# Performance work log

Measured on AMD Instinct MI355X. Metric: run time of the kernel, lower is better.

The kernel has to match this reference:

```python
import jax, jax.numpy as jnp
import numpy as np

B, C, D, H, W = 8, 96, 8, 32, 32
HW, DIM, NH = H * W, C * D, 4
DH = DIM // NH
EPS_NORM = 1e-12
EPS_LN = 1e-5


def setup_inputs() -> dict:
    key = jax.random.key(0)
    ks = jax.random.split(key, 10)
    s = 0.02
    return {
        "x": jax.random.normal(ks[0], (B, C, D, H, W), jnp.float32),
        "pos_embed": jax.random.normal(ks[1], (1, HW, DIM), jnp.float32) * s,
        "qkv_w": jax.random.normal(ks[2], (3 * DIM, DIM), jnp.float32) * s,
        "proj_w": jax.random.normal(ks[3], (DIM, DIM), jnp.float32) * s,
        "proj_b": jnp.zeros((DIM,), jnp.float32),
        "temperature": jnp.ones((NH, 1, 1), jnp.float32),
        "ln_gamma": jnp.ones((DIM,), jnp.float32),
        "ln_beta": jnp.zeros((DIM,), jnp.float32),
        "dw_w": jax.random.normal(ks[4], (C, 1, 3, 3, 3), jnp.float32) * s,
        "dw_b": jnp.zeros((C,), jnp.float32),
        "pw_w": jax.random.normal(ks[5], (C, C, 1, 1, 1), jnp.float32) * s,
        "pw_b": jnp.zeros((C,), jnp.float32),
    }


def _l2norm_seq(t):
    # normalize over the HW axis (dim=-2), matching F.normalize(dim=-2)
    n = jnp.sqrt(jnp.sum(t * t, axis=-2, keepdims=True))
    return t / jnp.maximum(n, EPS_NORM)


def _dsconv(y, dw_w, dw_b, pw_w, pw_b):
    dn = ("NCDHW", "OIDHW", "NCDHW")
    z = jax.lax.conv_general_dilated(y, dw_w, (1, 1, 1), [(1, 1)] * 3,
                                     dimension_numbers=dn, feature_group_count=C)
    z = z + dw_b[None, :, None, None, None]
    z = jax.lax.conv_general_dilated(z, pw_w, (1, 1, 1), [(0, 0)] * 3,
                                     dimension_numbers=dn)
    return z + pw_b[None, :, None, None, None]


def reference(x, pos_embed, qkv_w, proj_w, proj_b, temperature,
              ln_gamma, ln_beta, dw_w, dw_b, pw_w, pw_b):
    save = x
    # b c d h w -> b (h w) (c d)
    t = jnp.transpose(x, (0, 3, 4, 1, 2)).reshape(B, HW, DIM)
    t = t + pos_embed
    # qkv projection (no bias)
    qkv = (t @ qkv_w.T).reshape(B, HW, 3, NH, DH)
    qkv = jnp.transpose(qkv, (2, 0, 3, 1, 4))  # [3,B,NH,HW,DH]
    q, k, v = qkv[0], qkv[1], qkv[2]
    q = _l2norm_seq(q)
    k = _l2norm_seq(k)
    attn = jnp.einsum("bhnd,bhmd->bhnm", q, k) * temperature  # temp broadcasts [NH,1,1]
    attn = jax.nn.softmax(attn, axis=-1)  # dropout = identity at eval
    o = jnp.einsum("bhnm,bhmd->bhnd", attn, v)
    o = jnp.transpose(o, (0, 2, 1, 3)).reshape(B, HW, DIM)
    o = o @ proj_w.T + proj_b
    # LayerNorm applied to attention output
    mu = jnp.mean(o, axis=-1, keepdims=True)
    var = jnp.mean((o - mu) ** 2, axis=-1, keepdims=True)
    o = (o - mu) / jnp.sqrt(var + EPS_LN) * ln_gamma + ln_beta
    # b (h w) (c d) -> b c d h w
    o = o.reshape(B, H, W, C, D)
    o = jnp.transpose(o, (0, 3, 4, 1, 2))
    y = o + save
    return y + _dsconv(y, dw_w, dw_b, pw_w, pw_b)
```

## Files before the change

### kernel.cpp

```cpp
#include <hip/hip_runtime.h>

typedef unsigned short u16;
typedef unsigned int u32;

typedef __attribute__((ext_vector_type(8))) short short8;
typedef __attribute__((ext_vector_type(4))) float floatx4;

__device__ __forceinline__ float bf2f(u16 u) { return __uint_as_float(((u32)u) << 16); }
__device__ __forceinline__ u16 f2bf(float f) {
    u32 x = __float_as_uint(f);
    x += 0x7fffu + ((x >> 16) & 1u);
    return (u16)(x >> 16);
}
__device__ __forceinline__ void gl_lds16(const void* g, void* l) {
    __builtin_amdgcn_global_load_lds((const __attribute__((address_space(1))) u32*)g,
                                     (__attribute__((address_space(3))) u32*)l, 16, 0, 0);
}


__global__ __launch_bounds__(256) void k_init(const float* __restrict__ x,
                                              const float* __restrict__ pos,
                                              const float* __restrict__ wq,
                                              const float* __restrict__ wp,
                                              const float* __restrict__ wpw,
                                              u16* __restrict__ t,
                                              u16* __restrict__ wout,
                                              float* __restrict__ zbuf) {
    __shared__ float tile[64][65];
    const int bid = blockIdx.x;
    const int tid = threadIdx.x;
    if (bid < 1536) {
        const int cd0 = (bid % 12) * 64;
        const int hw0 = ((bid / 12) & 15) * 64;
        const int b = bid / 192;
#pragma unroll
        for (int i = 0; i < 16; i++) {
            int f = i * 256 + tid;
            int cdl = f >> 6, hwl = f & 63;
            int cd = cd0 + cdl, c = cd >> 3, d = cd & 7;
            tile[cdl][hwl] = x[(size_t)(((b * 96 + c) * 8 + d)) * 1024 + hw0 + hwl];
        }
        __syncthreads();
#pragma unroll
        for (int it = 0; it < 2; it++) {
            int u = it * 256 + tid;
            int ch = u >> 6, l = u & 63;
            int n16l = ch >> 1, kcl = ch & 1;
            int hwl = n16l * 16 + (l & 15);
            int cdl = kcl * 32 + (l >> 4) * 8;
            int row = b * 1024 + hw0 + hwl;
            int cd = cd0 + cdl;
            const float* pp = pos + (size_t)(hw0 + hwl) * 768 + cd;
            float4 p0 = *(const float4*)pp;
            float4 p1 = *(const float4*)(pp + 4);
            short8 v;
            v[0] = (short)f2bf(tile[cdl + 0][hwl] + p0.x);
            v[1] = (short)f2bf(tile[cdl + 1][hwl] + p0.y);
            v[2] = (short)f2bf(tile[cdl + 2][hwl] + p0.z);
            v[3] = (short)f2bf(tile[cdl + 3][hwl] + p0.w);
            v[4] = (short)f2bf(tile[cdl + 4][hwl] + p1.x);
            v[5] = (short)f2bf(tile[cdl + 5][hwl] + p1.y);
            v[6] = (short)f2bf(tile[cdl + 6][hwl] + p1.z);
            v[7] = (short)f2bf(tile[cdl + 7][hwl] + p1.w);
            size_t chunk = (size_t)(row >> 4) * 24 + (cd >> 5);
            *(short8*)(t + chunk * 512 + l * 8) = v;
        }
    } else if (bid < 2724) {
        const int NQ = 144 * 24 * 64;
        const int NP = NQ + 48 * 24 * 64;
        int u = (bid - 1536) * 256 + tid;
        if (u < NP) {
            const float* w = (u < NQ) ? wq : wp;
            int ub = (u < NQ) ? u : u - NQ;
            int chunk = ub >> 6, l = ub & 63;
            int n16 = chunk / 24, kc = chunk - n16 * 24;
            int n = n16 * 16 + (l & 15);
            int k0 = kc * 32 + (l >> 4) * 8;
            const float* src = w + (size_t)n * 768 + k0;
            float4 a = *(const float4*)src;
            float4 b2 = *(const float4*)(src + 4);
            short8 v;
            v[0] = (short)f2bf(a.x);  v[1] = (short)f2bf(a.y);
            v[2] = (short)f2bf(a.z);  v[3] = (short)f2bf(a.w);
            v[4] = (short)f2bf(b2.x); v[5] = (short)f2bf(b2.y);
            v[6] = (short)f2bf(b2.z); v[7] = (short)f2bf(b2.w);
            *(short8*)(wout + (size_t)u * 8) = v;
        } else {
            int i = u - NP;
            wout[(size_t)NP * 8 + i] = f2bf(wpw[i]);
        }
    } else {
        int i = (bid - 2724) * 256 + tid;
        zbuf[i] = 0.f;
    }
}

template <int MODE>
__global__ __launch_bounds__(256) void gemm_bt(const u16* __restrict__ A,
                                               const u16* __restrict__ Bw,
                                               int M, int N, int K,
                                               u16* __restrict__ qo, u16* __restrict__ ko,
                                               u16* __restrict__ vo,
                                               const float* __restrict__ bias,
                                               u16* __restrict__ Co,
                                               float* __restrict__ sqa,
                                               float* __restrict__ ska,
                                               float* __restrict__ musum,
                                               float* __restrict__ sqsum) {
    __shared__ __align__(16) u16 lAB[128 * 136];
    u16* lA = lAB;
    u16* lB = lAB + 16 * 512;
    const int tid = threadIdx.x;
    const int lane = tid & 63;
    const int wv = tid >> 6;
    const int wr = wv >> 1, wc = wv & 1;
    const int ntiles = N >> 7;
    const int mtiles = M >> 7;
    const int lin = blockIdx.x;
    const int xcd = lin & 7;
    const int idx = lin >> 3;
    const int mlocal = idx / ntiles;
    const int ntile = idx - mlocal * ntiles;
    const int m0 = (xcd * (mtiles >> 3) + mlocal) << 7;
    const int n0 = ntile << 7;
    const int lr = lane & 15;
    const int lq = lane >> 4;

    floatx4 acc[4][4];
#pragma unroll
    for (int i = 0; i < 4; i++)
#pragma unroll
        for (int j = 0; j < 4; j++) acc[i][j] = (floatx4){0.f, 0.f, 0.f, 0.f};

    const int m16 = m0 >> 4, n16 = n0 >> 4;
    for (int kc2 = 0; kc2 < (K >> 6); kc2++) {
        __syncthreads();
#pragma unroll
        for (int kh = 0; kh < 2; kh++) {
#pragma unroll
            for (int i = 0; i < 2; i++) {
                int ch16 = i * 4 + wv;
                int kc = kc2 * 2 + kh;
                const u16* ga = A + ((size_t)(m16 + ch16) * 24 + kc) * 512 + lane * 8;
                gl_lds16(ga, (char*)lA + (kh * 8 + ch16) * 1024);
                const u16* gb = Bw + ((size_t)(n16 + ch16) * 24 + kc) * 512 + lane * 8;
                gl_lds16(gb, (char*)lB + (kh * 8 + ch16) * 1024);
            }
        }
        __syncthreads();
#pragma unroll
        for (int kh = 0; kh < 2; kh++) {
            short8 af[4], bfr[4];
#pragma unroll
            for (int tt = 0; tt < 4; tt++) {
                af[tt] = *(const short8*)(lA + ((kh * 8 + wr * 4 + tt) * 64 + lane) * 8);
                bfr[tt] = *(const short8*)(lB + ((kh * 8 + wc * 4 + tt) * 64 + lane) * 8);
            }
#pragma unroll
            for (int mt = 0; mt < 4; mt++)
#pragma unroll
                for (int nt = 0; nt < 4; nt++)
                    acc[mt][nt] = __builtin_amdgcn_mfma_f32_16x16x32_bf16(af[mt], bfr[nt], acc[mt][nt], 0, 0, 0);
        }
    }

    if (MODE == 0) {
        const int region = n0 / 768;
        const int n0r = n0 - region * 768;
        const int bb0 = m0 >> 10;
        if (region < 2) {
            float* dst = (region == 0) ? sqa : ska;
#pragma unroll
            for (int nt = 0; nt < 4; nt++) {
                int colb = n0r + wc * 64 + nt * 16;
                int h = colb / 192;
                int dh = colb - h * 192 + lr;
                float s = 0.f;
#pragma unroll
                for (int mt = 0; mt < 4; mt++)
#pragma unroll
                    for (int r = 0; r < 4; r++) s += acc[mt][nt][r] * acc[mt][nt][r];
                s += __shfl_xor(s, 16);
                s += __shfl_xor(s, 32);
                if (lq == 0) atomicAdd(&dst[(bb0 * 4 + h) * 192 + dh], s);
            }
        }
        __syncthreads();
        if (region < 2) {
#pragma unroll
            for (int nt = 0; nt < 4; nt++) {
                int lch = wc * 2 + (nt >> 1);
                int offbase = (((nt & 1) * 2 + (lr >> 3)) * 16) * 8 + (lr & 7);
#pragma unroll
                for (int mt = 0; mt < 4; mt++) {
                    u16* cp2 = lAB + (((wr * 4 + mt) * 4 + lch) * 512);
#pragma unroll
                    for (int r = 0; r < 4; r++)
                        cp2[offbase + (lq * 4 + r) * 8] = f2bf(acc[mt][nt][r]);
                }
            }
        } else {
#pragma unroll
            for (int nt = 0; nt < 4; nt++) {
#pragma unroll
                for (int mt = 0; mt < 4; mt++) {
                    u16* cp2 = lAB + (((wr * 2 + (mt >> 1)) * 8 + wc * 4 + nt) * 512);
                    int ob = (((mt & 1) * 2 + (lq >> 1)) * 16 + lr) * 8 + (lq & 1) * 4;
#pragma unroll
                    for (int r = 0; r < 4; r++)
                        cp2[ob + r] = f2bf(acc[mt][nt][r]);
                }
            }
        }
        __syncthreads();
        const int b = m0 >> 10;
        const int ml = m0 & 1023;
        u16* dsto = (region == 0) ? qo : (region == 1) ? ko : vo;
#pragma unroll
        for (int i = 0; i < 8; i++) {
            int ci = wv * 8 + i;
            short8 val = *(const short8*)(lAB + ci * 512 + lane * 8);
            if (region < 2) {
                int a = ci >> 2, bb = ci & 3;
                int cg = n0r + bb * 32;
                int h = cg / 192;
                int dh32 = (cg - h * 192) >> 5;
                size_t gaddr = (size_t)(b * 4 + h) * 196608 +
                               (size_t)((((ml >> 4) + a) * 6 + dh32)) * 512 + lane * 8;
                *(short8*)(dsto + gaddr) = val;
            } else {
                int a = ci >> 3, bb = ci & 7;
                int cg = n0r + bb * 16;
                int h = cg / 192;
                int dh16 = (cg - h * 192) >> 4;
                size_t gaddr = (size_t)(b * 4 + h) * 196608 +
                               (size_t)((((ml >> 5) + a) * 12 + dh16)) * 512 + lane * 8;
                *(short8*)(dsto + gaddr) = val;
            }
        }
    } else {
        float bvv[4];
#pragma unroll
        for (int nt = 0; nt < 4; nt++) bvv[nt] = bias[n0 + wc * 64 + nt * 16 + lr];
#pragma unroll
        for (int mt = 0; mt < 4; mt++) {
#pragma unroll
            for (int r = 0; r < 4; r++) {
                float s = 0.f, ss = 0.f;
#pragma unroll
                for (int nt = 0; nt < 4; nt++) {
                    float v = acc[mt][nt][r] + bvv[nt];
                    s += v;
                    ss += v * v;
                }
#pragma unroll
                for (int m = 1; m < 16; m <<= 1) {
                    s += __shfl_xor(s, m);
                    ss += __shfl_xor(ss, m);
                }
                if (lr == 0) {
                    int row = m0 + wr * 64 + mt * 16 + lq * 4 + r;
                    atomicAdd(&musum[row], s);
                    atomicAdd(&sqsum[row], ss);
                }
            }
        }
        __syncthreads();
#pragma unroll
        for (int nt = 0; nt < 4; nt++) {
            int coll = wc * 64 + nt * 16 + lr;
#pragma unroll
            for (int mt = 0; mt < 4; mt++) {
#pragma unroll
                for (int r = 0; r < 4; r++) {
                    int rowl = wr * 64 + mt * 16 + lq * 4 + r;
                    lAB[rowl * 136 + coll] = f2bf(acc[mt][nt][r] + bvv[nt]);
                }
            }
        }
        __syncthreads();
#pragma unroll
        for (int i = 0; i < 8; i++) {
            int u = i * 256 + tid;
            int rowl = u >> 4, l = u & 15;
            short8 val = *(const short8*)(lAB + rowl * 136 + l * 8);
            *(short8*)(Co + (size_t)(m0 + rowl) * N + n0 + l * 8) = val;
        }
    }
}

__global__ __launch_bounds__(128) void k_attn(const u16* __restrict__ q,
                                              const u16* __restrict__ kmat,
                                              const u16* __restrict__ vT,
                                              const float* __restrict__ sqq,
                                              const float* __restrict__ sqk,
                                              const float* __restrict__ temp,
                                              u16* __restrict__ o) {
    __shared__ __align__(16) u16 lK[24 * 512];
    __shared__ __align__(16) u16 lV[24 * 512];
    __shared__ __align__(16) u16 lP[2 * 2048];
    __shared__ float lcs[192];
    const int lin = blockIdx.x;
    const int qb = (lin >> 3) & 15;
    const int bh = (lin & 7) * 4 + (lin >> 7);
    const int b = bh >> 2, h = bh & 3;
    const int tid = threadIdx.x;
    const int lane = tid & 63;
    const int wv = tid >> 6;
    const int lr = lane & 15;
    const int lq = lane >> 4;
    const int koff = lq * 8;

    const u16* qbase = q + (size_t)bh * 196608;
    const u16* kbase = kmat + (size_t)bh * 196608;
    const u16* vbase = vT + (size_t)bh * 196608;

    {
        const float tv = temp[bh & 3];
        for (int i = tid; i < 192; i += 128) {
            float rq = 1.f / fmaxf(sqrtf(sqq[bh * 192 + i]), 1e-12f);
            float rk = 1.f / fmaxf(sqrtf(sqk[bh * 192 + i]), 1e-12f);
            lcs[i] = rq * rk * tv;
        }
    }
    __syncthreads();

    short8 qf[2][6];
#pragma unroll
    for (int t = 0; t < 2; t++) {
        const int qr16 = qb * 4 + wv * 2 + t;
#pragma unroll
        for (int ks = 0; ks < 6; ks++) {
            short8 raw = *(const short8*)(qbase + ((size_t)(qr16 * 6 + ks)) * 512 + (size_t)lane * 8);
            short8 sc;
#pragma unroll
            for (int j = 0; j < 8; j++) {
                float f = bf2f((u16)raw[j]) * lcs[ks * 32 + koff + j];
                sc[j] = (short)f2bf(f);
            }
            qf[t][ks] = sc;
        }
    }

    float l_r[2][4];
    floatx4 oacc[2][12];
#pragma unroll
    for (int t = 0; t < 2; t++) {
#pragma unroll
        for (int r = 0; r < 4; r++) l_r[t][r] = 0.f;
#pragma unroll
        for (int vt = 0; vt < 12; vt++) oacc[t][vt] = (floatx4){0.f, 0.f, 0.f, 0.f};
    }

    u16* lp = lP + wv * 2048;

    auto stage_K = [&](int kb2) {
#pragma unroll
        for (int i = 0; i < 12; i++) {
            int ch = i * 2 + wv;
            int ks = ch >> 2, nt = ch & 3;
            const u16* gk = kbase + ((size_t)(kb2 * 4 + nt) * 6 + ks) * 512 + lane * 8;
            gl_lds16(gk, (char*)lK + ch * 1024);
        }
    };
    auto stage_V = [&](int kb2) {
#pragma unroll
        for (int i = 0; i < 12; i++) {
            int ch = i * 2 + wv;
            int ks2 = ch / 12, vt2 = ch - ks2 * 12;
            const u16* gv = vbase + ((size_t)(kb2 * 2 + ks2) * 12 + vt2) * 512 + lane * 8;
            gl_lds16(gv, (char*)lV + ch * 1024);
        }
    };

    asm volatile("s_waitcnt vmcnt(0)" ::: "memory");
    stage_K(0);
    stage_V(0);
    asm volatile("s_waitcnt vmcnt(12)" ::: "memory");
    __builtin_amdgcn_s_barrier();

    for (int kb = 0; kb < 16; kb++) {
        floatx4 s0[4], s1[4];
#pragma unroll
        for (int nt = 0; nt < 4; nt++) {
            s0[nt] = (floatx4){0.f, 0.f, 0.f, 0.f};
            s1[nt] = (floatx4){0.f, 0.f, 0.f, 0.f};
        }
        __builtin_amdgcn_s_setprio(1);
#pragma unroll
        for (int ks = 0; ks < 6; ks++) {
#pragma unroll
            for (int nt = 0; nt < 4; nt++) {
                short8 kf = *(const short8*)(lK + ((ks * 4 + nt) * 64 + lane) * 8);
                s0[nt] = __builtin_amdgcn_mfma_f32_16x16x32_bf16(qf[0][ks], kf, s0[nt], 0, 0, 0);
                s1[nt] = __builtin_amdgcn_mfma_f32_16x16x32_bf16(qf[1][ks], kf, s1[nt], 0, 0, 0);
            }
        }
        __builtin_amdgcn_s_setprio(0);
        __builtin_amdgcn_s_barrier();
        if (kb < 15) stage_K(kb + 1);

        float rs0[4] = {0.f, 0.f, 0.f, 0.f}, rs1[4] = {0.f, 0.f, 0.f, 0.f};
#pragma unroll
        for (int nt = 0; nt < 4; nt++)
#pragma unroll
            for (int r = 0; r < 4; r++) {
                float p0 = __expf(s0[nt][r]);
                s0[nt][r] = p0;
                rs0[r] += p0;
                float p1 = __expf(s1[nt][r]);
                s1[nt][r] = p1;
                rs1[r] += p1;
            }
#pragma unroll
        for (int m = 1; m < 16; m <<= 1)
#pragma unroll
            for (int r = 0; r < 4; r++) {
                rs0[r] += __shfl_xor(rs0[r], m);
                rs1[r] += __shfl_xor(rs1[r], m);
            }
#pragma unroll
        for (int r = 0; r < 4; r++) {
            l_r[0][r] += rs0[r];
            l_r[1][r] += rs1[r];
        }
#pragma unroll
        for (int nt = 0; nt < 4; nt++) {
            int base2 = (nt >> 1) * 512 + ((nt & 1) * 2 + (lr >> 3)) * 128 + (lr & 7);
#pragma unroll
            for (int r = 0; r < 4; r++) {
                lp[base2 + (lq * 4 + r) * 8] = f2bf(s0[nt][r]);
                lp[1024 + base2 + (lq * 4 + r) * 8] = f2bf(s1[nt][r]);
            }
        }

        if (kb < 15) { asm volatile("s_waitcnt vmcnt(12)" ::: "memory"); }
        else         { asm volatile("s_waitcnt vmcnt(0)" ::: "memory"); }
        __builtin_amdgcn_s_barrier();

        __builtin_amdgcn_s_setprio(1);
#pragma unroll
        for (int ks2 = 0; ks2 < 2; ks2++) {
            short8 pf0 = *(const short8*)(lp + ks2 * 512 + lane * 8);
            short8 pf1 = *(const short8*)(lp + 1024 + ks2 * 512 + lane * 8);
#pragma unroll
            for (int vt = 0; vt < 12; vt++) {
                short8 vf = *(const short8*)(lV + ((ks2 * 12 + vt) * 64 + lane) * 8);
                oacc[0][vt] = __builtin_amdgcn_mfma_f32_16x16x32_bf16(pf0, vf, oacc[0][vt], 0, 0, 0);
                oacc[1][vt] = __builtin_amdgcn_mfma_f32_16x16x32_bf16(pf1, vf, oacc[1][vt], 0, 0, 0);
            }
        }
        __builtin_amdgcn_s_setprio(0);
        __builtin_amdgcn_s_barrier();
        if (kb < 15) {
            stage_V(kb + 1);
            asm volatile("s_waitcnt vmcnt(12)" ::: "memory");
            __builtin_amdgcn_s_barrier();
        }
    }

    __syncthreads();
#pragma unroll
    for (int t = 0; t < 2; t++) {
        float inv[4];
#pragma unroll
        for (int r = 0; r < 4; r++) inv[r] = 1.f / l_r[t][r];
#pragma unroll
        for (int vt = 0; vt < 12; vt++) {
            int col = vt * 16 + lr;
            int swb = (col >> 5) * 512 + (((col >> 3) & 3) * 16) * 8 + (col & 7);
#pragma unroll
            for (int r = 0; r < 4; r++) {
                int rowl = wv * 32 + t * 16 + lq * 4 + r;
                lK[(rowl >> 4) * 3072 + swb + (rowl & 15) * 8] = f2bf(oacc[t][vt][r] * inv[r]);
            }
        }
    }
    __syncthreads();
#pragma unroll
    for (int i = 0; i < 12; i++) {
        int u = i * 128 + tid;
        int chl = u >> 6, l = u & 63;
        short8 val = *(const short8*)(lK + chl * 512 + l * 8);
        int a = chl / 6, kc = chl - a * 6;
        size_t gaddr = ((size_t)(b * 64 + qb * 4 + a) * 24 + h * 6 + kc) * 512 + l * 8;
        *(short8*)(o + gaddr) = val;
    }
}

__global__ __launch_bounds__(256) void k_lnt(const u16* __restrict__ o2,
                                             const float* __restrict__ musum,
                                             const float* __restrict__ sqsum,
                                             const float* __restrict__ gamma,
                                             const float* __restrict__ beta,
                                             const float* __restrict__ x,
                                             float* __restrict__ y) {
    __shared__ float tile[64][65];
    const int b = blockIdx.z, hw0 = blockIdx.y * 64, cd0 = blockIdx.x * 64;
    const int tid = threadIdx.x;
#pragma unroll
    for (int i = 0; i < 16; i++) {
        int f = i * 256 + tid;
        int hwl = f >> 6, cdl = f & 63;
        int row = b * 1024 + hw0 + hwl;
        float m_ = musum[row] * (1.f / 768.f);
        float var = fmaxf(sqsum[row] * (1.f / 768.f) - m_ * m_, 0.f);
        float rstd = rsqrtf(var + 1e-5f);
        float v = bf2f(o2[(size_t)row * 768 + cd0 + cdl]);
        v = (v - m_) * rstd * gamma[cd0 + cdl] + beta[cd0 + cdl];
        tile[hwl][cdl] = v;
    }
    __syncthreads();
#pragma unroll
    for (int i = 0; i < 16; i++) {
        int f = i * 256 + tid;
        int cdl = f >> 6, hwl = f & 63;
        int cd = cd0 + cdl, c = cd >> 3, d = cd & 7;
        size_t addr = (size_t)((b * 96 + c) * 8 + d) * 1024 + hw0 + hwl;
        y[addr] = tile[hwl][cdl] + x[addr];
    }
}

__global__ __launch_bounds__(256) void k_dw(const float* __restrict__ y,
                                            const float* __restrict__ w,
                                            const float* __restrict__ bias,
                                            u16* __restrict__ z) {
    __shared__ float ly[8192];
    const int bc = blockIdx.x;
    const int c = bc % 96;
    const int tid = threadIdx.x;
    const size_t base = (size_t)bc * 8192;

#pragma unroll
    for (int i = 0; i < 8; i++) {
        int i4 = i * 256 + tid;
        *(float4*)(ly + i4 * 4) = *(const float4*)(y + base + i4 * 4);
    }
    float wt[27];
#pragma unroll
    for (int j = 0; j < 27; j++) wt[j] = w[c * 27 + j];
    const float bv = bias[c];
    __syncthreads();

    const int wcol = tid & 31;
    const int hh = tid >> 5;

    for (int hb = 0; hb < 4; hb++) {
        const int h = hb * 8 + hh;
        float pl[3][9];
        auto loadplane = [&](int dd, float* p) {
#pragma unroll
            for (int kh = 0; kh < 3; kh++) {
                int h2 = h + kh - 1;
                bool hok = (unsigned)h2 < 32u;
                const float* row = ly + dd * 1024 + h2 * 32;
#pragma unroll
                for (int kw = 0; kw < 3; kw++) {
                    int w2 = wcol + kw - 1;
                    bool ok = hok && (unsigned)w2 < 32u;
                    p[kh * 3 + kw] = ok ? row[w2] : 0.f;
                }
            }
        };
#pragma unroll
        for (int j = 0; j < 9; j++) pl[0][j] = 0.f;
        loadplane(0, pl[1]);
#pragma unroll
        for (int d = 0; d < 8; d++) {
            if (d < 7) loadplane(d + 1, pl[2]);
            else {
#pragma unroll
                for (int j = 0; j < 9; j++) pl[2][j] = 0.f;
            }
            float acc = bv;
#pragma unroll
            for (int kd = 0; kd < 3; kd++)
#pragma unroll
                for (int j = 0; j < 9; j++) acc += wt[kd * 9 + j] * pl[kd][j];
            z[base + d * 1024 + h * 32 + wcol] = f2bf(acc);
#pragma unroll
            for (int j = 0; j < 9; j++) { pl[0][j] = pl[1][j]; pl[1][j] = pl[2][j]; }
        }
    }
}

__global__ __launch_bounds__(256) void k_pw(const u16* __restrict__ z,
                                            const u16* __restrict__ wbf,
                                            const float* __restrict__ bias,
                                            float* __restrict__ out) {
    __shared__ __align__(16) u16 lZ[128 * 104];
    __shared__ __align__(16) u16 lW[96 * 104];
    const int tid = threadIdx.x;
    const int lane = tid & 63;
    const int wv = tid >> 6;
    const int lr = lane & 15;
    const int lq = lane >> 4;
    const int koff = lq * 8;

    const int idx = blockIdx.x;
    const int q = idx & 7;
    const int bd = idx >> 3;
    const int b = bd >> 3, d = bd & 7;
    const int pos0 = q * 128;

    for (int i = tid; i < 96 * 96; i += 256) {
        int row = i / 96, col = i - row * 96;
        lW[row * 104 + col] = wbf[i];
    }
    {
        const int pos = tid & 127;
        const int cc0 = (tid >> 7) * 48;
        const size_t gbase = ((size_t)b * 96 * 8 + d) * 1024 + pos0 + pos;
#pragma unroll
        for (int g = 0; g < 6; g++) {
            short8 v;
#pragma unroll
            for (int j = 0; j < 8; j++) {
                int cc = cc0 + g * 8 + j;
                v[j] = (short)z[gbase + (size_t)cc * 8192];
            }
            *(short8*)(lZ + pos * 104 + cc0 + g * 8) = v;
        }
    }
    __syncthreads();

    floatx4 acc[6][2];
#pragma unroll
    for (int m = 0; m < 6; m++)
#pragma unroll
        for (int nt = 0; nt < 2; nt++) acc[m][nt] = (floatx4){0.f, 0.f, 0.f, 0.f};

#pragma unroll
    for (int ks = 0; ks < 3; ks++) {
        short8 bfrg[2];
#pragma unroll
        for (int nt = 0; nt < 2; nt++)
            bfrg[nt] = *(const short8*)(lZ + (wv * 32 + nt * 16 + lr) * 104 + ks * 32 + koff);
#pragma unroll
        for (int m = 0; m < 6; m++) {
            short8 afr = *(const short8*)(lW + (m * 16 + lr) * 104 + ks * 32 + koff);
#pragma unroll
            for (int nt = 0; nt < 2; nt++)
                acc[m][nt] = __builtin_amdgcn_mfma_f32_16x16x32_bf16(afr, bfrg[nt], acc[m][nt], 0, 0, 0);
        }
    }

#pragma unroll
    for (int m = 0; m < 6; m++) {
#pragma unroll
        for (int r = 0; r < 4; r++) {
            int c = m * 16 + lq * 4 + r;
            float bv = bias[c];
            size_t rowbase = ((size_t)(b * 96 + c) * 8 + d) * 1024 + pos0;
#pragma unroll
            for (int nt = 0; nt < 2; nt++) {
                int pos = wv * 32 + nt * 16 + lr;
                size_t a = rowbase + pos;
                out[a] = out[a] + bv + acc[m][nt][r];
            }
        }
    }
}

extern "C" void kernel_launch(void* const* d_in, const int* in_sizes, int n_in,
                              void* d_out, int out_size, void* d_ws, size_t ws_size,
                              hipStream_t stream) {
    (void)in_sizes; (void)n_in; (void)out_size; (void)ws_size;
    const float* x      = (const float*)d_in[0];
    const float* pos    = (const float*)d_in[1];
    const float* qkv_w  = (const float*)d_in[2];
    const float* proj_w = (const float*)d_in[3];
    const float* proj_b = (const float*)d_in[4];
    const float* temp   = (const float*)d_in[5];
    const float* ln_g   = (const float*)d_in[6];
    const float* ln_b   = (const float*)d_in[7];
    const float* dw_w   = (const float*)d_in[8];
    const float* dw_b   = (const float*)d_in[9];
    const float* pw_w   = (const float*)d_in[10];
    const float* pw_b   = (const float*)d_in[11];
    float* out = (float*)d_out;
    char* ws = (char*)d_ws;

    u16* t    = (u16*)(ws + 0);
    u16* vT   = (u16*)(ws + 12582912);
    u16* q    = (u16*)(ws + 25165824);
    u16* kk   = (u16*)(ws + 37748736);
    u16* wqb  = (u16*)(ws + 50331648);
    float* sqq   = (float*)(ws + 55175168);
    float* sqk   = (float*)(ws + 55199744);
    float* musum = (float*)(ws + 55224320);
    float* sqsum = (float*)(ws + 55257088);
    u16* wpb  = wqb + 2304 * 768;
    u16* wpwb = wqb + 2304 * 768 + 768 * 768;
    u16* o   = t;
    u16* o2  = q;
    u16* z   = t;
    float* y  = out;

    k_init<<<2836, 256, 0, stream>>>(x, pos, qkv_w, proj_w, pw_w, t, wqb, sqq);
    gemm_bt<0><<<1152, 256, 0, stream>>>(t, wqb, 8192, 2304, 768, q, kk, vT, nullptr, nullptr,
                                         sqq, sqk, nullptr, nullptr);
    k_attn<<<512, 128, 0, stream>>>(q, kk, vT, sqq, sqk, temp, o);
    gemm_bt<1><<<384, 256, 0, stream>>>(o, wpb, 8192, 768, 768, nullptr, nullptr, nullptr, proj_b,
                                        o2, nullptr, nullptr, musum, sqsum);
    k_lnt<<<dim3(12, 16, 8), 256, 0, stream>>>(o2, musum, sqsum, ln_g, ln_b, x, y);
    k_dw<<<768, 256, 0, stream>>>(y, dw_w, dw_b, z);
    k_pw<<<512, 256, 0, stream>>>(z, wpwb, pw_b, out);
}
```

Measured before the change: 261.1 us.

## Split attention block across four waves with one query tile per wave

The attention kernel now launches 256 threads (four waves) per block instead of two. Each wave handles one 16-row query tile instead of two. Staging of K and V tiles is spread over four waves, and the wait counts and output write loop are adjusted to match. This cuts per-wave register pressure (the accumulator set is halved) and adds more waves to hide latency, at the cost of reusing each loaded K/V fragment for only one MFMA per wave and running more barriers per unit of work.

```diff
diff --git a/kernel.cpp b/kernel.cpp
--- a/kernel.cpp
+++ b/kernel.cpp
@@ -289,7 +289,7 @@
     }
 }
 
-__global__ __launch_bounds__(128) void k_attn(const u16* __restrict__ q,
+__global__ __launch_bounds__(256) void k_attn(const u16* __restrict__ q,
                                               const u16* __restrict__ kmat,
                                               const u16* __restrict__ vT,
                                               const float* __restrict__ sqq,
@@ -298,7 +298,7 @@
                                               u16* __restrict__ o) {
     __shared__ __align__(16) u16 lK[24 * 512];
     __shared__ __align__(16) u16 lV[24 * 512];
-    __shared__ __align__(16) u16 lP[2 * 2048];
+    __shared__ __align__(16) u16 lP[4 * 1024];
     __shared__ float lcs[192];
     const int lin = blockIdx.x;
     const int qb = (lin >> 3) & 15;
@@ -317,7 +317,7 @@
 
     {
         const float tv = temp[bh & 3];
-        for (int i = tid; i < 192; i += 128) {
+        for (int i = tid; i < 192; i += 256) {
             float rq = 1.f / fmaxf(sqrtf(sqq[bh * 192 + i]), 1e-12f);
             float rk = 1.f / fmaxf(sqrtf(sqk[bh * 192 + i]), 1e-12f);
             lcs[i] = rq * rk * tv;
@@ -325,10 +325,9 @@
     }
     __syncthreads();
 
-    short8 qf[2][6];
-#pragma unroll
-    for (int t = 0; t < 2; t++) {
-        const int qr16 = qb * 4 + wv * 2 + t;
+    short8 qf[6];
+    {
+        const int qr16 = qb * 4 + wv;
 #pragma unroll
         for (int ks = 0; ks < 6; ks++) {
             short8 raw = *(const short8*)(qbase + ((size_t)(qr16 * 6 + ks)) * 512 + (size_t)lane * 8);
@@ -338,26 +337,23 @@
                 float f = bf2f((u16)raw[j]) * lcs[ks * 32 + koff + j];
                 sc[j] = (short)f2bf(f);
             }
-            qf[t][ks] = sc;
-        }
-    }
-
-    float l_r[2][4];
-    floatx4 oacc[2][12];
-#pragma unroll
-    for (int t = 0; t < 2; t++) {
-#pragma unroll
-        for (int r = 0; r < 4; r++) l_r[t][r] = 0.f;
-#pragma unroll
-        for (int vt = 0; vt < 12; vt++) oacc[t][vt] = (floatx4){0.f, 0.f, 0.f, 0.f};
-    }
-
-    u16* lp = lP + wv * 2048;
+            qf[ks] = sc;
+        }
+    }
+
+    float l_r[4];
+    floatx4 oacc[12];
+#pragma unroll
+    for (int r = 0; r < 4; r++) l_r[r] = 0.f;
+#pragma unroll
+    for (int vt = 0; vt < 12; vt++) oacc[vt] = (floatx4){0.f, 0.f, 0.f, 0.f};
+
+    u16* lp = lP + wv * 1024;
 
     auto stage_K = [&](int kb2) {
 #pragma unroll
-        for (int i = 0; i < 12; i++) {
-            int ch = i * 2 + wv;
+        for (int i = 0; i < 6; i++) {
+            int ch = i * 4 + wv;
             int ks = ch >> 2, nt = ch & 3;
             const u16* gk = kbase + ((size_t)(kb2 * 4 + nt) * 6 + ks) * 512 + lane * 8;
             gl_lds16(gk, (char*)lK + ch * 1024);
@@ -365,8 +361,8 @@
     };
     auto stage_V = [&](int kb2) {
 #pragma unroll
-        for (int i = 0; i < 12; i++) {
-            int ch = i * 2 + wv;
+        for (int i = 0; i < 6; i++) {
+            int ch = i * 4 + wv;
             int ks2 = ch / 12, vt2 = ch - ks2 * 12;
             const u16* gv = vbase + ((size_t)(kb2 * 2 + ks2) * 12 + vt2) * 512 + lane * 8;
             gl_lds16(gv, (char*)lV + ch * 1024);
@@ -376,31 +372,27 @@
     asm volatile("s_waitcnt vmcnt(0)" ::: "memory");
     stage_K(0);
     stage_V(0);
-    asm volatile("s_waitcnt vmcnt(12)" ::: "memory");
+    asm volatile("s_waitcnt vmcnt(6)" ::: "memory");
     __builtin_amdgcn_s_barrier();
 
     for (int kb = 0; kb < 16; kb++) {
-        floatx4 s0[4], s1[4];
-#pragma unroll
-        for (int nt = 0; nt < 4; nt++) {
-            s0[nt] = (floatx4){0.f, 0.f, 0.f, 0.f};
-            s1[nt] = (floatx4){0.f, 0.f, 0.f, 0.f};
-        }
+        floatx4 s0[4];
+#pragma unroll
+        for (int nt = 0; nt < 4; nt++) s0[nt] = (floatx4){0.f, 0.f, 0.f, 0.f};
         __builtin_amdgcn_s_setprio(1);
 #pragma unroll
         for (int ks = 0; ks < 6; ks++) {
 #pragma unroll
             for (int nt = 0; nt < 4; nt++) {
                 short8 kf = *(const short8*)(lK + ((ks * 4 + nt) * 64 + lane) * 8);
-                s0[nt] = __builtin_amdgcn_mfma_f32_16x16x32_bf16(qf[0][ks], kf, s0[nt], 0, 0, 0);
-                s1[nt] = __builtin_amdgcn_mfma_f32_16x16x32_bf16(qf[1][ks], kf, s1[nt], 0, 0, 0);
+                s0[nt] = __builtin_amdgcn_mfma_f32_16x16x32_bf16(qf[ks], kf, s0[nt], 0, 0, 0);
             }
         }
         __builtin_amdgcn_s_setprio(0);
         __builtin_amdgcn_s_barrier();
         if (kb < 15) stage_K(kb + 1);
 
-        float rs0[4] = {0.f, 0.f, 0.f, 0.f}, rs1[4] = {0.f, 0.f, 0.f, 0.f};
+        float rs0[4] = {0.f, 0.f, 0.f, 0.f};
 #pragma unroll
         for (int nt = 0; nt < 4; nt++)
 #pragma unroll
@@ -408,33 +400,22 @@
                 float p0 = __expf(s0[nt][r]);
                 s0[nt][r] = p0;
                 rs0[r] += p0;
-                float p1 = __expf(s1[nt][r]);
-                s1[nt][r] = p1;
-                rs1[r] += p1;
             }
 #pragma unroll
         for (int m = 1; m < 16; m <<= 1)
 #pragma unroll
-            for (int r = 0; r < 4; r++) {
-                rs0[r] += __shfl_xor(rs0[r], m);
-                rs1[r] += __shfl_xor(rs1[r], m);
-            }
-#pragma unroll
-        for (int r = 0; r < 4; r++) {
-            l_r[0][r] += rs0[r];
-            l_r[1][r] += rs1[r];
-        }
+            for (int r = 0; r < 4; r++) rs0[r] += __shfl_xor(rs0[r], m);
+#pragma unroll
+        for (int r = 0; r < 4; r++) l_r[r] += rs0[r];
 #pragma unroll
         for (int nt = 0; nt < 4; nt++) {
             int base2 = (nt >> 1) * 512 + ((nt & 1) * 2 + (lr >> 3)) * 128 + (lr & 7);
 #pragma unroll
-            for (int r = 0; r < 4; r++) {
+            for (int r = 0; r < 4; r++)
                 lp[base2 + (lq * 4 + r) * 8] = f2bf(s0[nt][r]);
-                lp[1024 + base2 + (lq * 4 + r) * 8] = f2bf(s1[nt][r]);
-            }
-        }
-
-        if (kb < 15) { asm volatile("s_waitcnt vmcnt(12)" ::: "memory"); }
+        }
+
+        if (kb < 15) { asm volatile("s_waitcnt vmcnt(6)" ::: "memory"); }
         else         { asm volatile("s_waitcnt vmcnt(0)" ::: "memory"); }
         __builtin_amdgcn_s_barrier();
 
@@ -442,44 +423,41 @@
 #pragma unroll
         for (int ks2 = 0; ks2 < 2; ks2++) {
             short8 pf0 = *(const short8*)(lp + ks2 * 512 + lane * 8);
-            short8 pf1 = *(const short8*)(lp + 1024 + ks2 * 512 + lane * 8);
 #pragma unroll
             for (int vt = 0; vt < 12; vt++) {
                 short8 vf = *(const short8*)(lV + ((ks2 * 12 + vt) * 64 + lane) * 8);
-                oacc[0][vt] = __builtin_amdgcn_mfma_f32_16x16x32_bf16(pf0, vf, oacc[0][vt], 0, 0, 0);
-                oacc[1][vt] = __builtin_amdgcn_mfma_f32_16x16x32_bf16(pf1, vf, oacc[1][vt], 0, 0, 0);
+                oacc[vt] = __builtin_amdgcn_mfma_f32_16x16x32_bf16(pf0, vf, oacc[vt], 0, 0, 0);
             }
         }
         __builtin_amdgcn_s_setprio(0);
         __builtin_amdgcn_s_barrier();
         if (kb < 15) {
             stage_V(kb + 1);
-            asm volatile("s_waitcnt vmcnt(12)" ::: "memory");
+            asm volatile("s_waitcnt vmcnt(6)" ::: "memory");
             __builtin_amdgcn_s_barrier();
         }
     }
 
     __syncthreads();
-#pragma unroll
-    for (int t = 0; t < 2; t++) {
+    {
         float inv[4];
 #pragma unroll
-        for (int r = 0; r < 4; r++) inv[r] = 1.f / l_r[t][r];
+        for (int r = 0; r < 4; r++) inv[r] = 1.f / l_r[r];
 #pragma unroll
         for (int vt = 0; vt < 12; vt++) {
             int col = vt * 16 + lr;
             int swb = (col >> 5) * 512 + (((col >> 3) & 3) * 16) * 8 + (col & 7);
 #pragma unroll
             for (int r = 0; r < 4; r++) {
-                int rowl = wv * 32 + t * 16 + lq * 4 + r;
-                lK[(rowl >> 4) * 3072 + swb + (rowl & 15) * 8] = f2bf(oacc[t][vt][r] * inv[r]);
+                int rowl = wv * 16 + lq * 4 + r;
+                lK[(rowl >> 4) * 3072 + swb + (rowl & 15) * 8] = f2bf(oacc[vt][r] * inv[r]);
             }
         }
     }
     __syncthreads();
 #pragma unroll
-    for (int i = 0; i < 12; i++) {
-        int u = i * 128 + tid;
+    for (int i = 0; i < 6; i++) {
+        int u = i * 256 + tid;
         int chl = u >> 6, l = u & 63;
         short8 val = *(const short8*)(lK + chl * 512 + l * 8);
         int a = chl / 6, kc = chl - a * 6;
@@ -700,7 +678,7 @@
     k_init<<<2836, 256, 0, stream>>>(x, pos, qkv_w, proj_w, pw_w, t, wqb, sqq);
     gemm_bt<0><<<1152, 256, 0, stream>>>(t, wqb, 8192, 2304, 768, q, kk, vT, nullptr, nullptr,
                                          sqq, sqk, nullptr, nullptr);
-    k_attn<<<512, 128, 0, stream>>>(q, kk, vT, sqq, sqk, temp, o);
+    k_attn<<<512, 256, 0, stream>>>(q, kk, vT, sqq, sqk, temp, o);
     gemm_bt<1><<<384, 256, 0, stream>>>(o, wpb, 8192, 768, 768, nullptr, nullptr, nullptr, proj_b,
                                         o2, nullptr, nullptr, musum, sqsum);
     k_lnt<<<dim3(12, 16, 8), 256, 0, stream>>>(o2, musum, sqsum, ln_g, ln_b, x, y);
```

Result: faster. 251.1 us (median of 2 runs) (-3.8%).
